# Kernel optimization log

Hardware: AMD Instinct MI355X
Metric: run time of the kernel (lower is better)

The kernel has to match this reference:

```python
import jax, jax.numpy as jnp
import numpy as np

N_NODES = 100000
IN_CH = 256
EMBED = 256
N_EDGES = 300000
EPS = 1e-5


def _glorot(key, shape):
    fan_in, fan_out = shape[0], shape[1]
    lim = (6.0 / (fan_in + fan_out)) ** 0.5
    return jax.random.uniform(key, shape, jnp.float32, -lim, lim)


def setup_inputs() -> dict:
    key = jax.random.key(0)
    ks = jax.random.split(key, 16)
    inp = {}
    inp['node_feat'] = jax.random.normal(ks[0], (N_NODES, IN_CH), jnp.float32)
    inp['src'] = jax.random.randint(ks[1], (N_EDGES,), 0, N_NODES, jnp.int32)
    inp['dst'] = jax.random.randint(ks[2], (N_EDGES,), 0, N_NODES, jnp.int32)
    inp['neg'] = jax.random.randint(ks[3], (N_EDGES,), 0, N_NODES, jnp.int32)
    # GCNConv weights (x @ W + b), 3 layers
    inp['W1'] = _glorot(ks[4], (IN_CH, EMBED)); inp['b1'] = jnp.zeros((EMBED,), jnp.float32)
    inp['W2'] = _glorot(ks[5], (EMBED, EMBED)); inp['b2'] = jnp.zeros((EMBED,), jnp.float32)
    inp['W3'] = _glorot(ks[6], (EMBED, EMBED)); inp['b3'] = jnp.zeros((EMBED,), jnp.float32)
    # BatchNorm affine params (2 BN layers)
    inp['g1'] = jnp.ones((EMBED,), jnp.float32); inp['be1'] = jnp.zeros((EMBED,), jnp.float32)
    inp['g2'] = jnp.ones((EMBED,), jnp.float32); inp['be2'] = jnp.zeros((EMBED,), jnp.float32)
    # LinkPredictor MLP
    inp['fc1_w'] = _glorot(ks[7], (2 * EMBED, EMBED)); inp['fc1_b'] = jnp.zeros((EMBED,), jnp.float32)
    inp['fc2_w'] = _glorot(ks[8], (EMBED, 1)); inp['fc2_b'] = jnp.zeros((1,), jnp.float32)
    return inp


def gcn_conv(x, W, b, src, dst, n):
    # PyG GCNConv: out = D^{-1/2} (A + I) D^{-1/2} (x @ W) + b
    xw = x @ W
    loops = jnp.arange(n, dtype=src.dtype)
    src_l = jnp.concatenate([src, loops])
    dst_l = jnp.concatenate([dst, loops])
    deg = jax.ops.segment_sum(jnp.ones_like(dst_l, jnp.float32), dst_l, num_segments=n)
    dinv = jnp.where(deg > 0, jax.lax.rsqrt(deg), 0.0)
    norm = dinv[src_l] * dinv[dst_l]  # [E+N]
    msg = norm[:, None] * xw[src_l]   # [E+N, d]
    out = jax.ops.segment_sum(msg, dst_l, num_segments=n)
    return out + b


def batch_norm(x, g, b):
    # training-mode BN over node dim, biased variance (torch semantics)
    mu = jnp.mean(x, axis=0)
    var = jnp.mean((x - mu) ** 2, axis=0)
    return (x - mu) * jax.lax.rsqrt(var + EPS) * g + b


def link_pred(z_a, z_b, fc1_w, fc1_b, fc2_w, fc2_b):
    h = jnp.concatenate([z_a, z_b], axis=1) @ fc1_w + fc1_b
    h = jax.nn.relu(h)
    return jax.nn.sigmoid(h @ fc2_w + fc2_b).reshape(-1)


def reference(node_feat, src, dst, neg, W1, b1, W2, b2, W3, b3, g1, be1, g2, be2, fc1_w, fc1_b, fc2_w, fc2_b):
    n = node_feat.shape[0]
    # encoder (dropout p used only in training; inference/deterministic here)
    x = gcn_conv(node_feat, W1, b1, src, dst, n)
    x = jax.nn.relu(batch_norm(x, g1, be1))
    x = gcn_conv(x, W2, b2, src, dst, n)
    x = jax.nn.relu(batch_norm(x, g2, be2))
    z = gcn_conv(x, W3, b3, src, dst, n)
    z_src, z_dst, z_neg = z[src], z[dst], z[neg]
    pos_out = link_pred(z_src, z_dst, fc1_w, fc1_b, fc2_w, fc2_b)
    neg_out = link_pred(z_src, z_neg, fc1_w, fc1_b, fc2_w, fc2_b)
    return (pos_out, neg_out)
```

## Files before the change

kernel.cpp:

```cpp
#include <hip/hip_runtime.h>
#include <hip/hip_bf16.h>

#define N_NODES 100000
#define N_EDGES 300000
#define CH 256
#define EPS 1e-5f
#define AGG_BLOCKS 3125
#define Y_TILES 782
#define Y_TILES_PAD 784

typedef __hip_bfloat16 bf16;
typedef __attribute__((ext_vector_type(8))) short bf16x8_t;
typedef __attribute__((ext_vector_type(4))) float f32x4_t;

__device__ __forceinline__ unsigned short f2bf(float f) {
    bf16 h = __float2bfloat16(f);
    return __builtin_bit_cast(unsigned short, h);
}
__device__ __forceinline__ float bf2f(unsigned short u) {
    unsigned int x = ((unsigned int)u) << 16;
    return __builtin_bit_cast(float, x);
}
__device__ __forceinline__ float bflo(unsigned int w) {
    return __builtin_bit_cast(float, w << 16);
}
__device__ __forceinline__ float bfhi(unsigned int w) {
    return __builtin_bit_cast(float, w & 0xffff0000u);
}
__device__ __forceinline__ unsigned pack2(float a, float b) {
    return (unsigned)f2bf(a) | ((unsigned)f2bf(b) << 16);
}
__device__ __forceinline__ void store_val(bf16* p, float v) { *p = __float2bfloat16(v); }

__device__ __forceinline__ void async_copy16(const void* g, void* l) {
    __builtin_amdgcn_global_load_lds((const __attribute__((address_space(1))) void*)g,
                                     (__attribute__((address_space(3))) void*)l, 16, 0, 0);
}

__global__ void k_zero_int(int* __restrict__ p, int n) {
    int i = blockIdx.x * 256 + threadIdx.x;
    if (i < n) p[i] = 0;
}
__global__ void k_count_deg(const int* __restrict__ dst, int* __restrict__ deg) {
    int e = blockIdx.x * 256 + threadIdx.x;
    if (e < N_EDGES) atomicAdd(&deg[dst[e]], 1);
}
__global__ void k_dinv_from_deg(const int* __restrict__ deg, float* __restrict__ dinv) {
    int i = blockIdx.x * 256 + threadIdx.x;
    if (i < N_NODES) dinv[i] = rsqrtf((float)(deg[i] + 1));
}
__global__ void k_block_sums(const int* __restrict__ deg, int* __restrict__ bsum) {
    __shared__ int s[256];
    int t = threadIdx.x;
    int i = blockIdx.x * 256 + t;
    s[t] = (i < N_NODES) ? deg[i] : 0;
    __syncthreads();
    for (int off = 128; off > 0; off >>= 1) {
        if (t < off) s[t] += s[t + off];
        __syncthreads();
    }
    if (t == 0) bsum[blockIdx.x] = s[0];
}
__global__ void k_scan_bsums(int* __restrict__ bsum, int nb) {
    __shared__ int s[512];
    int t = threadIdx.x;
    int v = (t < nb) ? bsum[t] : 0;
    s[t] = v;
    __syncthreads();
    for (int off = 1; off < 512; off <<= 1) {
        int u = (t >= off) ? s[t - off] : 0;
        __syncthreads();
        s[t] += u;
        __syncthreads();
    }
    if (t < nb) bsum[t] = s[t] - v;
}
__global__ void k_row_ptr(const int* __restrict__ deg, const int* __restrict__ bsum,
                          int* __restrict__ row_ptr) {
    __shared__ int s[256];
    int t = threadIdx.x;
    int i = blockIdx.x * 256 + t;
    int v = (i < N_NODES) ? deg[i] : 0;
    s[t] = v;
    __syncthreads();
    for (int off = 1; off < 256; off <<= 1) {
        int u = (t >= off) ? s[t - off] : 0;
        __syncthreads();
        s[t] += u;
        __syncthreads();
    }
    if (i < N_NODES) row_ptr[i] = bsum[blockIdx.x] + s[t] - v;
    if (blockIdx.x == 0 && t == 0) row_ptr[N_NODES] = N_EDGES;
}
__global__ void k_scatter(const int* __restrict__ src, const int* __restrict__ dst,
                          const int* __restrict__ row_ptr, int* __restrict__ cursor,
                          const float* __restrict__ dinv,
                          int* __restrict__ col, float* __restrict__ wedge,
                          int* __restrict__ eid, int* __restrict__ rowid) {
    int e = blockIdx.x * 256 + threadIdx.x;
    if (e < N_EDGES) {
        int d = dst[e], s = src[e];
        int p = atomicAdd(&cursor[d], 1);
        int idx = row_ptr[d] + p;
        col[idx] = s;
        wedge[idx] = dinv[d] * dinv[s];
        eid[idx] = e;
        rowid[idx] = d;
    }
}

__global__ void k_transpose_all(const float* __restrict__ W1, const float* __restrict__ W2,
                                const float* __restrict__ W3, const float* __restrict__ fc1w,
                                bf16* __restrict__ wt) {
    int which = blockIdx.x >> 8;
    int idx = ((blockIdx.x & 255) << 8) + threadIdx.x;
    int n = idx >> 8, k = idx & 255;
    const float* W; int ro = 0;
    switch (which) {
        case 0: W = W1; break;
        case 1: W = W2; break;
        case 2: W = W3; break;
        case 3: W = fc1w; break;
        default: W = fc1w; ro = 256; break;
    }
    wt[(size_t)which * 65536 + (size_t)n * 256 + k] =
        __float2bfloat16(W[(size_t)(ro + k) * 256 + n]);
}

__global__ void k_cast_bf16_v4(const float* __restrict__ x, unsigned short* __restrict__ y) {
    int i = blockIdx.x * 256 + threadIdx.x;
    float4 v = ((const float4*)x)[i];
    ushort4 o;
    o.x = f2bf(v.x); o.y = f2bf(v.y); o.z = f2bf(v.z); o.w = f2bf(v.w);
    ((ushort4*)y)[i] = o;
}
__global__ void k_bn_relu_bf16(unsigned short* __restrict__ x, const float* __restrict__ scale,
                               const float* __restrict__ shift) {
    int i = blockIdx.x * 256 + threadIdx.x;
    ushort4 m = ((ushort4*)x)[i];
    int c = (i & 63) * 4;
    float4 sc = *(const float4*)(scale + c);
    float4 sh = *(const float4*)(shift + c);
    ushort4 o;
    o.x = f2bf(fmaxf(bf2f(m.x) * sc.x + sh.x, 0.f));
    o.y = f2bf(fmaxf(bf2f(m.y) * sc.y + sh.y, 0.f));
    o.z = f2bf(fmaxf(bf2f(m.z) * sc.z + sh.z, 0.f));
    o.w = f2bf(fmaxf(bf2f(m.w) * sc.w + sh.w, 0.f));
    ((ushort4*)x)[i] = o;
}

template <int NX, bool BIAS>
__global__ __launch_bounds__(256) void k_gemm_mfma(const bf16* __restrict__ A,
                                                   const bf16* __restrict__ Bt,
                                                   bf16* __restrict__ C, int M, int ldc,
                                                   const float* __restrict__ bias256) {
    constexpr int LOG2NX = (NX == 4) ? 2 : 1;
    int id = blockIdx.x;
    int rg = (id & 7) + 8 * (id >> (3 + LOG2NX));
    int ct = (id >> 3) & (NX - 1);
    if (rg >= Y_TILES) return;
    const int row0 = rg * 128;
    const int col0 = ct * 128;

    __shared__ bf16 As[128 * 64];
    __shared__ bf16 Bs[128 * 64];
    const int tid = threadIdx.x;
    const int lane = tid & 63;
    const int w = tid >> 6;
    const int wr = w >> 1, wc = w & 1;
    const int lr = lane & 15, quad = lane >> 4;

    f32x4_t acc[4][4] = {};

    for (int k0 = 0; k0 < 256; k0 += 64) {
#pragma unroll
        for (int i = 0; i < 4; ++i) {
            int j = i * 256 + tid;
            int r = j >> 3, c = j & 7;
            int gk = ((c ^ (r & 7)) << 3);
            int gr = row0 + r; gr = gr < M ? gr : M - 1;
            async_copy16(A + (size_t)gr * 256 + k0 + gk, (void*)(As + j * 8));
            async_copy16(Bt + (size_t)(col0 + r) * 256 + k0 + gk, (void*)(Bs + j * 8));
        }
        __syncthreads();
#pragma unroll
        for (int ks = 0; ks < 2; ++ks) {
            bf16x8_t af[4], bfr[4];
#pragma unroll
            for (int mi = 0; mi < 4; ++mi) {
                int m = wr * 64 + mi * 16 + lr;
                int c = (ks * 4 + quad) ^ (m & 7);
                af[mi] = *(const bf16x8_t*)(As + m * 64 + c * 8);
            }
#pragma unroll
            for (int ni = 0; ni < 4; ++ni) {
                int n = wc * 64 + ni * 16 + lr;
                int c = (ks * 4 + quad) ^ (n & 7);
                bfr[ni] = *(const bf16x8_t*)(Bs + n * 64 + c * 8);
            }
#pragma unroll
            for (int mi = 0; mi < 4; ++mi)
#pragma unroll
                for (int ni = 0; ni < 4; ++ni)
                    acc[mi][ni] = __builtin_amdgcn_mfma_f32_16x16x32_bf16(
                        af[mi], bfr[ni], acc[mi][ni], 0, 0, 0);
        }
        __syncthreads();
    }
    float bv[4];
#pragma unroll
    for (int ni = 0; ni < 4; ++ni) {
        int colg = col0 + wc * 64 + ni * 16 + lr;
        bv[ni] = (BIAS && colg < 256) ? bias256[colg] : 0.f;
    }
#pragma unroll
    for (int mi = 0; mi < 4; ++mi) {
#pragma unroll
        for (int r = 0; r < 4; ++r) {
            int row = row0 + wr * 64 + mi * 16 + quad * 4 + r;
            if (row < M) {
#pragma unroll
                for (int ni = 0; ni < 4; ++ni) {
                    int colg = col0 + wc * 64 + ni * 16 + lr;
                    store_val(C + (size_t)row * ldc + colg, acc[mi][ni][r] + bv[ni]);
                }
            }
        }
    }
}

template <bool STATS>
__global__ __launch_bounds__(256) void k_agg_csr(const unsigned short* __restrict__ xw,
                                                 const int* __restrict__ row_ptr,
                                                 const int* __restrict__ col,
                                                 const float* __restrict__ wedge,
                                                 const float* __restrict__ dinv,
                                                 const float* __restrict__ bias,
                                                 bf16* __restrict__ out,
                                                 float* __restrict__ part) {
    __shared__ float sred[8][256];
    __shared__ float qred[8][256];
    int g = threadIdx.x >> 5, lh = threadIdx.x & 31;
    int base = blockIdx.x * 32 + g * 4;
    const uint4* xwv = (const uint4*)xw;
    float4 b0 = ((const float4*)bias)[lh * 2];
    float4 b1 = ((const float4*)bias)[lh * 2 + 1];
    float s8[8] = {}, q8[8] = {};
#pragma unroll
    for (int n = 0; n < 4; ++n) {
        int node = base + n;
        int beg = row_ptr[node], end = row_ptr[node + 1];
        float dv = dinv[node];
        uint4 xr = xwv[(size_t)node * 32 + lh];
        float s2 = dv * dv;
        float a0 = s2 * bflo(xr.x), a1 = s2 * bfhi(xr.x);
        float a2 = s2 * bflo(xr.y), a3 = s2 * bfhi(xr.y);
        float a4 = s2 * bflo(xr.z), a5 = s2 * bfhi(xr.z);
        float a6 = s2 * bflo(xr.w), a7 = s2 * bfhi(xr.w);
        int i = beg;
        for (; i + 2 <= end; i += 2) {
            int sa = col[i], sb = col[i + 1];
            float wa = wedge[i], wb = wedge[i + 1];
            uint4 ma = xwv[(size_t)sa * 32 + lh];
            uint4 mb = xwv[(size_t)sb * 32 + lh];
            a0 += wa * bflo(ma.x) + wb * bflo(mb.x);
            a1 += wa * bfhi(ma.x) + wb * bfhi(mb.x);
            a2 += wa * bflo(ma.y) + wb * bflo(mb.y);
            a3 += wa * bfhi(ma.y) + wb * bfhi(mb.y);
            a4 += wa * bflo(ma.z) + wb * bflo(mb.z);
            a5 += wa * bfhi(ma.z) + wb * bfhi(mb.z);
            a6 += wa * bflo(ma.w) + wb * bflo(mb.w);
            a7 += wa * bfhi(ma.w) + wb * bfhi(mb.w);
        }
        if (i < end) {
            int sa = col[i];
            float wa = wedge[i];
            uint4 ma = xwv[(size_t)sa * 32 + lh];
            a0 += wa * bflo(ma.x); a1 += wa * bfhi(ma.x);
            a2 += wa * bflo(ma.y); a3 += wa * bfhi(ma.y);
            a4 += wa * bflo(ma.z); a5 += wa * bfhi(ma.z);
            a6 += wa * bflo(ma.w); a7 += wa * bfhi(ma.w);
        }
        a0 += b0.x; a1 += b0.y; a2 += b0.z; a3 += b0.w;
        a4 += b1.x; a5 += b1.y; a6 += b1.z; a7 += b1.w;
        uint4 o;
        o.x = pack2(a0, a1); o.y = pack2(a2, a3);
        o.z = pack2(a4, a5); o.w = pack2(a6, a7);
        ((uint4*)(out + (size_t)node * CH))[lh] = o;
        if (STATS) {
            s8[0] += a0; s8[1] += a1; s8[2] += a2; s8[3] += a3;
            s8[4] += a4; s8[5] += a5; s8[6] += a6; s8[7] += a7;
            q8[0] += a0 * a0; q8[1] += a1 * a1; q8[2] += a2 * a2; q8[3] += a3 * a3;
            q8[4] += a4 * a4; q8[5] += a5 * a5; q8[6] += a6 * a6; q8[7] += a7 * a7;
        }
    }
    if (STATS) {
#pragma unroll
        for (int j = 0; j < 8; ++j) {
            sred[g][lh * 8 + j] = s8[j];
            qred[g][lh * 8 + j] = q8[j];
        }
        __syncthreads();
        int t = threadIdx.x;
        float ss = 0.f, qq = 0.f;
#pragma unroll
        for (int gg = 0; gg < 8; ++gg) {
            ss += sred[gg][t];
            qq += qred[gg][t];
        }
        part[(size_t)blockIdx.x * 512 + t] = ss;
        part[(size_t)blockIdx.x * 512 + 256 + t] = qq;
    }
}

__global__ __launch_bounds__(256) void k_bn_finalize(const float* __restrict__ part,
                                                     const float* __restrict__ g,
                                                     const float* __restrict__ be,
                                                     float* __restrict__ scale,
                                                     float* __restrict__ shift) {
    int wave = threadIdx.x >> 6, lane = threadIdx.x & 63;
    int c = blockIdx.x * 4 + wave;
    float s = 0.f, q = 0.f;
    for (int j = lane; j < AGG_BLOCKS; j += 64) {
        s += part[(size_t)j * 512 + c];
        q += part[(size_t)j * 512 + 256 + c];
    }
#pragma unroll
    for (int off = 32; off > 0; off >>= 1) {
        s += __shfl_down(s, off, 64);
        q += __shfl_down(q, off, 64);
    }
    if (lane == 0) {
        float mu = s * (1.0f / N_NODES);
        float var = q * (1.0f / N_NODES) - mu * mu;
        float sc = g[c] * rsqrtf(var + EPS);
        scale[c] = sc;
        shift[c] = be[c] - mu * sc;
    }
}

__global__ __launch_bounds__(256) void k_edge_score(
        const unsigned short* __restrict__ uv,
        const int* __restrict__ col, const int* __restrict__ eid,
        const int* __restrict__ rowid, const int* __restrict__ neg,
        const float* __restrict__ fc2_w, const float* __restrict__ fc2_b,
        float* __restrict__ out) {
    constexpr int NWG = 18750;
    constexpr int Q = NWG / 8, R = NWG % 8;
    int bid = blockIdx.x;
    int xcd = bid & 7, ord = bid >> 3;
    int swz = ((xcd < R) ? xcd * (Q + 1) : R * (Q + 1) + (xcd - R) * Q) + ord;
    int wave = threadIdx.x >> 6, lane = threadIdx.x & 63;
    int qtr = lane >> 4, l = lane & 15;
    int i = swz * 16 + wave * 4 + qtr;
    int s = col[i], d = rowid[i], e = eid[i];
    int g = neg[e];
    const uint4* uvv = (const uint4*)uv;
    uint4 u0 = uvv[(size_t)s * 64 + l * 2];
    uint4 u1 = uvv[(size_t)s * 64 + l * 2 + 1];
    uint4 p0 = uvv[(size_t)d * 64 + 32 + l * 2];
    uint4 p1 = uvv[(size_t)d * 64 + 33 + l * 2];
    uint4 n0 = uvv[(size_t)g * 64 + 32 + l * 2];
    uint4 n1 = uvv[(size_t)g * 64 + 33 + l * 2];
    float4 w0 = ((const float4*)fc2_w)[l * 4];
    float4 w1 = ((const float4*)fc2_w)[l * 4 + 1];
    float4 w2 = ((const float4*)fc2_w)[l * 4 + 2];
    float4 w3 = ((const float4*)fc2_w)[l * 4 + 3];

    float t0 = bflo(u0.x), t1 = bfhi(u0.x), t2 = bflo(u0.y), t3 = bfhi(u0.y);
    float t4 = bflo(u0.z), t5 = bfhi(u0.z), t6 = bflo(u0.w), t7 = bfhi(u0.w);
    float t8 = bflo(u1.x), t9 = bfhi(u1.x), ta = bflo(u1.y), tb = bfhi(u1.y);
    float tc = bflo(u1.z), td = bfhi(u1.z), te = bflo(u1.w), tf = bfhi(u1.w);

    float accp =
        fmaxf(t0 + bflo(p0.x), 0.f) * w0.x + fmaxf(t1 + bfhi(p0.x), 0.f) * w0.y +
        fmaxf(t2 + bflo(p0.y), 0.f) * w0.z + fmaxf(t3 + bfhi(p0.y), 0.f) * w0.w +
        fmaxf(t4 + bflo(p0.z), 0.f) * w1.x + fmaxf(t5 + bfhi(p0.z), 0.f) * w1.y +
        fmaxf(t6 + bflo(p0.w), 0.f) * w1.z + fmaxf(t7 + bfhi(p0.w), 0.f) * w1.w +
        fmaxf(t8 + bflo(p1.x), 0.f) * w2.x + fmaxf(t9 + bfhi(p1.x), 0.f) * w2.y +
        fmaxf(ta + bflo(p1.y), 0.f) * w2.z + fmaxf(tb + bfhi(p1.y), 0.f) * w2.w +
        fmaxf(tc + bflo(p1.z), 0.f) * w3.x + fmaxf(td + bfhi(p1.z), 0.f) * w3.y +
        fmaxf(te + bflo(p1.w), 0.f) * w3.z + fmaxf(tf + bfhi(p1.w), 0.f) * w3.w;
    float accn =
        fmaxf(t0 + bflo(n0.x), 0.f) * w0.x + fmaxf(t1 + bfhi(n0.x), 0.f) * w0.y +
        fmaxf(t2 + bflo(n0.y), 0.f) * w0.z + fmaxf(t3 + bfhi(n0.y), 0.f) * w0.w +
        fmaxf(t4 + bflo(n0.z), 0.f) * w1.x + fmaxf(t5 + bfhi(n0.z), 0.f) * w1.y +
        fmaxf(t6 + bflo(n0.w), 0.f) * w1.z + fmaxf(t7 + bfhi(n0.w), 0.f) * w1.w +
        fmaxf(t8 + bflo(n1.x), 0.f) * w2.x + fmaxf(t9 + bfhi(n1.x), 0.f) * w2.y +
        fmaxf(ta + bflo(n1.y), 0.f) * w2.z + fmaxf(tb + bfhi(n1.y), 0.f) * w2.w +
        fmaxf(tc + bflo(n1.z), 0.f) * w3.x + fmaxf(td + bfhi(n1.z), 0.f) * w3.y +
        fmaxf(te + bflo(n1.w), 0.f) * w3.z + fmaxf(tf + bfhi(n1.w), 0.f) * w3.w;
#pragma unroll
    for (int off = 8; off > 0; off >>= 1) {
        accp += __shfl_down(accp, off, 64);
        accn += __shfl_down(accn, off, 64);
    }
    if (l == 0) {
        float bb = fc2_b[0];
        out[e] = 1.0f / (1.0f + expf(-(accp + bb)));
        out[N_EDGES + e] = 1.0f / (1.0f + expf(-(accn + bb)));
    }
}

extern "C" void kernel_launch(void* const* d_in, const int* in_sizes, int n_in,
                              void* d_out, int out_size, void* d_ws, size_t ws_size,
                              hipStream_t stream) {
    const float* node_feat = (const float*)d_in[0];
    const int* src = (const int*)d_in[1];
    const int* dst = (const int*)d_in[2];
    const int* neg = (const int*)d_in[3];
    const float* W1 = (const float*)d_in[4];  const float* b1 = (const float*)d_in[5];
    const float* W2 = (const float*)d_in[6];  const float* b2 = (const float*)d_in[7];
    const float* W3 = (const float*)d_in[8];  const float* b3 = (const float*)d_in[9];
    const float* g1 = (const float*)d_in[10]; const float* be1 = (const float*)d_in[11];
    const float* g2 = (const float*)d_in[12]; const float* be2 = (const float*)d_in[13];
    const float* fc1_w = (const float*)d_in[14]; const float* fc1_b = (const float*)d_in[15];
    const float* fc2_w = (const float*)d_in[16]; const float* fc2_b = (const float*)d_in[17];
    float* out = (float*)d_out;

    const size_t NF = (size_t)N_NODES * CH;
    bf16* UV = (bf16*)d_ws;
    bf16* Xbf = UV + 2 * NF;
    bf16* XwBf = Xbf + NF;
    bf16* wt = XwBf + NF;
    float* dinv = (float*)(wt + 5 * 65536);
    float* bnpart = dinv + N_NODES;
    float* scale = bnpart + (size_t)AGG_BLOCKS * 512;
    float* shift = scale + CH;
    float* wedge = shift + CH;
    int* ideg = (int*)(wedge + N_EDGES);
    int* cursor = ideg + N_NODES;
    int* row_ptr = cursor + N_NODES;
    int* col = row_ptr + N_NODES + 1;
    int* eid = col + N_EDGES;
    int* rowid = eid + N_EDGES;
    int* bsum = rowid + N_EDGES;
    (void)ws_size;

    int gemmBlocks = 2 * Y_TILES_PAD;
    int uvBlocks = 4 * Y_TILES_PAD;
    int nodeBlocks = (N_NODES + 255) / 256;
    int edgeBlocks = (N_EDGES + 255) / 256;
    int v4Blocks = (int)(NF / 4 / 256);
    int scoreBlocks = N_EDGES / 16;

    k_zero_int<<<(2 * N_NODES + 255) / 256, 256, 0, stream>>>(ideg, 2 * N_NODES);
    k_count_deg<<<edgeBlocks, 256, 0, stream>>>(dst, ideg);
    k_dinv_from_deg<<<nodeBlocks, 256, 0, stream>>>(ideg, dinv);
    k_block_sums<<<nodeBlocks, 256, 0, stream>>>(ideg, bsum);
    k_scan_bsums<<<1, 512, 0, stream>>>(bsum, nodeBlocks);
    k_row_ptr<<<nodeBlocks, 256, 0, stream>>>(ideg, bsum, row_ptr);
    k_scatter<<<edgeBlocks, 256, 0, stream>>>(src, dst, row_ptr, cursor, dinv, col, wedge,
                                              eid, rowid);

    k_transpose_all<<<1280, 256, 0, stream>>>(W1, W2, W3, fc1_w, wt);

    k_cast_bf16_v4<<<v4Blocks, 256, 0, stream>>>(node_feat, (unsigned short*)Xbf);
    k_gemm_mfma<2, false><<<gemmBlocks, 256, 0, stream>>>(Xbf, wt, XwBf, N_NODES, 256, nullptr);
    k_agg_csr<true><<<AGG_BLOCKS, 256, 0, stream>>>((unsigned short*)XwBf, row_ptr, col,
                                                    wedge, dinv, b1, Xbf, bnpart);
    k_bn_finalize<<<64, 256, 0, stream>>>(bnpart, g1, be1, scale, shift);
    k_bn_relu_bf16<<<v4Blocks, 256, 0, stream>>>((unsigned short*)Xbf, scale, shift);

    k_gemm_mfma<2, false><<<gemmBlocks, 256, 0, stream>>>(Xbf, wt + 65536, XwBf, N_NODES, 256, nullptr);
    k_agg_csr<true><<<AGG_BLOCKS, 256, 0, stream>>>((unsigned short*)XwBf, row_ptr, col,
                                                    wedge, dinv, b2, Xbf, bnpart);
    k_bn_finalize<<<64, 256, 0, stream>>>(bnpart, g2, be2, scale, shift);
    k_bn_relu_bf16<<<v4Blocks, 256, 0, stream>>>((unsigned short*)Xbf, scale, shift);

    k_gemm_mfma<2, false><<<gemmBlocks, 256, 0, stream>>>(Xbf, wt + 2 * 65536, XwBf, N_NODES, 256, nullptr);
    k_agg_csr<false><<<AGG_BLOCKS, 256, 0, stream>>>((unsigned short*)XwBf, row_ptr, col,
                                                     wedge, dinv, b3, Xbf, nullptr);

    k_gemm_mfma<4, true><<<uvBlocks, 256, 0, stream>>>(Xbf, wt + 3 * 65536, UV, N_NODES, 512, fc1_b);
    k_edge_score<<<scoreBlocks, 256, 0, stream>>>((unsigned short*)UV, col, eid, rowid, neg,
                                                  fc2_w, fc2_b, out);
}
```

Baseline: 632.5 us.

## Aggregate before GEMM, fuse BN stats into GEMM, fold W3 into fc1

Reorders each GCN layer to aggregate raw features first and then multiply by W, using linearity of the normalized adjacency. BatchNorm statistics are now computed in the GEMM epilogue, and the BN+ReLU is applied on the fly while gathering in the next aggregation, which removes the separate bn_relu pass. W3 is pre-multiplied into fc1 (and b3 folded into the bias), so the third GEMM and the UV GEMM become a single GEMM. The goal is fewer full passes over the 100k x 256 activations. In exchange, BN+ReLU is recomputed for every gathered neighbor and the different bf16 rounding order may shift numerics slightly.

```diff
diff --git a/kernel.cpp b/kernel.cpp
--- a/kernel.cpp
+++ b/kernel.cpp
@@ -110,21 +110,40 @@
 }
 
 __global__ void k_transpose_all(const float* __restrict__ W1, const float* __restrict__ W2,
-                                const float* __restrict__ W3, const float* __restrict__ fc1w,
                                 bf16* __restrict__ wt) {
     int which = blockIdx.x >> 8;
     int idx = ((blockIdx.x & 255) << 8) + threadIdx.x;
     int n = idx >> 8, k = idx & 255;
-    const float* W; int ro = 0;
-    switch (which) {
-        case 0: W = W1; break;
-        case 1: W = W2; break;
-        case 2: W = W3; break;
-        case 3: W = fc1w; break;
-        default: W = fc1w; ro = 256; break;
-    }
+    const float* W = which ? W2 : W1;
     wt[(size_t)which * 65536 + (size_t)n * 256 + k] =
-        __float2bfloat16(W[(size_t)(ro + k) * 256 + n]);
+        __float2bfloat16(W[(size_t)k * 256 + n]);
+}
+
+__global__ void k_fuse_w(const float* __restrict__ W3, const float* __restrict__ fc1w,
+                         bf16* __restrict__ wtf) {
+    __shared__ float w3row[256];
+    int k = blockIdx.x;
+    int n = threadIdx.x;
+    if (n < 256) w3row[n] = W3[(size_t)k * 256 + n];
+    __syncthreads();
+    int nc = n & 255;
+    size_t ro = (n < 256) ? 0 : 256;
+    float acc = 0.f;
+#pragma unroll 4
+    for (int j = 0; j < 256; ++j)
+        acc += w3row[j] * fc1w[(ro + j) * 256 + nc];
+    wtf[(size_t)n * 256 + k] = __float2bfloat16(acc);
+}
+__global__ void k_fuse_bias(const float* __restrict__ b3, const float* __restrict__ fc1w,
+                            const float* __restrict__ fc1b, float* __restrict__ bout) {
+    int n = threadIdx.x;
+    int nc = n & 255;
+    size_t ro = (n < 256) ? 0 : 256;
+    float acc = (n < 256) ? fc1b[n] : 0.f;
+#pragma unroll 4
+    for (int j = 0; j < 256; ++j)
+        acc += b3[j] * fc1w[(ro + j) * 256 + nc];
+    bout[n] = acc;
 }
 
 __global__ void k_cast_bf16_v4(const float* __restrict__ x, unsigned short* __restrict__ y) {
@@ -134,26 +153,13 @@
     o.x = f2bf(v.x); o.y = f2bf(v.y); o.z = f2bf(v.z); o.w = f2bf(v.w);
     ((ushort4*)y)[i] = o;
 }
-__global__ void k_bn_relu_bf16(unsigned short* __restrict__ x, const float* __restrict__ scale,
-                               const float* __restrict__ shift) {
-    int i = blockIdx.x * 256 + threadIdx.x;
-    ushort4 m = ((ushort4*)x)[i];
-    int c = (i & 63) * 4;
-    float4 sc = *(const float4*)(scale + c);
-    float4 sh = *(const float4*)(shift + c);
-    ushort4 o;
-    o.x = f2bf(fmaxf(bf2f(m.x) * sc.x + sh.x, 0.f));
-    o.y = f2bf(fmaxf(bf2f(m.y) * sc.y + sh.y, 0.f));
-    o.z = f2bf(fmaxf(bf2f(m.z) * sc.z + sh.z, 0.f));
-    o.w = f2bf(fmaxf(bf2f(m.w) * sc.w + sh.w, 0.f));
-    ((ushort4*)x)[i] = o;
-}
-
-template <int NX, bool BIAS>
+
+template <int NX, bool BIAS, bool STATS>
 __global__ __launch_bounds__(256) void k_gemm_mfma(const bf16* __restrict__ A,
                                                    const bf16* __restrict__ Bt,
                                                    bf16* __restrict__ C, int M, int ldc,
-                                                   const float* __restrict__ bias256) {
+                                                   const float* __restrict__ bias,
+                                                   float* __restrict__ part) {
     constexpr int LOG2NX = (NX == 4) ? 2 : 1;
     int id = blockIdx.x;
     int rg = (id & 7) + 8 * (id >> (3 + LOG2NX));
@@ -164,6 +170,8 @@
 
     __shared__ bf16 As[128 * 64];
     __shared__ bf16 Bs[128 * 64];
+    __shared__ float sS[2][128];
+    __shared__ float sQ[2][128];
     const int tid = threadIdx.x;
     const int lane = tid & 63;
     const int w = tid >> 6;
@@ -207,11 +215,54 @@
         }
         __syncthreads();
     }
-    float bv[4];
 #pragma unroll
     for (int ni = 0; ni < 4; ++ni) {
         int colg = col0 + wc * 64 + ni * 16 + lr;
-        bv[ni] = (BIAS && colg < 256) ? bias256[colg] : 0.f;
+        float bv = BIAS ? bias[colg] : 0.f;
+#pragma unroll
+        for (int mi = 0; mi < 4; ++mi)
+#pragma unroll
+            for (int r = 0; r < 4; ++r) acc[mi][ni][r] += bv;
+    }
+    if (STATS) {
+        float cs[4] = {}, cq[4] = {};
+#pragma unroll
+        for (int mi = 0; mi < 4; ++mi)
+#pragma unroll
+            for (int r = 0; r < 4; ++r) {
+                int row = row0 + wr * 64 + mi * 16 + quad * 4 + r;
+                if (row < M) {
+#pragma unroll
+                    for (int ni = 0; ni < 4; ++ni) {
+                        float v = acc[mi][ni][r];
+                        cs[ni] += v;
+                        cq[ni] += v * v;
+                    }
+                }
+            }
+#pragma unroll
+        for (int ni = 0; ni < 4; ++ni) {
+            cs[ni] += __shfl_xor(cs[ni], 16, 64);
+            cs[ni] += __shfl_xor(cs[ni], 32, 64);
+            cq[ni] += __shfl_xor(cq[ni], 16, 64);
+            cq[ni] += __shfl_xor(cq[ni], 32, 64);
+        }
+        if (quad == 0) {
+#pragma unroll
+            for (int ni = 0; ni < 4; ++ni) {
+                int cc = wc * 64 + ni * 16 + lr;
+                sS[wr][cc] = cs[ni];
+                sQ[wr][cc] = cq[ni];
+            }
+        }
+        __syncthreads();
+        if (tid < 128) {
+            float ss = sS[0][tid] + sS[1][tid];
+            float qq = sQ[0][tid] + sQ[1][tid];
+            int cg = col0 + tid;
+            part[(size_t)rg * 512 + cg] = ss;
+            part[(size_t)rg * 512 + 256 + cg] = qq;
+        }
     }
 #pragma unroll
     for (int mi = 0; mi < 4; ++mi) {
@@ -222,94 +273,83 @@
 #pragma unroll
                 for (int ni = 0; ni < 4; ++ni) {
                     int colg = col0 + wc * 64 + ni * 16 + lr;
-                    store_val(C + (size_t)row * ldc + colg, acc[mi][ni][r] + bv[ni]);
+                    store_val(C + (size_t)row * ldc + colg, acc[mi][ni][r]);
                 }
             }
         }
     }
 }
 
-template <bool STATS>
-__global__ __launch_bounds__(256) void k_agg_csr(const unsigned short* __restrict__ xw,
+template <bool BN>
+__device__ __forceinline__ void expand8(uint4 m, const float* sc, const float* sh, float* r) {
+    r[0] = bflo(m.x); r[1] = bfhi(m.x); r[2] = bflo(m.y); r[3] = bfhi(m.y);
+    r[4] = bflo(m.z); r[5] = bfhi(m.z); r[6] = bflo(m.w); r[7] = bfhi(m.w);
+    if (BN) {
+#pragma unroll
+        for (int i = 0; i < 8; ++i) r[i] = fmaxf(r[i] * sc[i] + sh[i], 0.f);
+    }
+}
+
+template <bool BN>
+__global__ __launch_bounds__(256) void k_agg_csr(const unsigned short* __restrict__ x,
                                                  const int* __restrict__ row_ptr,
                                                  const int* __restrict__ col,
                                                  const float* __restrict__ wedge,
                                                  const float* __restrict__ dinv,
-                                                 const float* __restrict__ bias,
-                                                 bf16* __restrict__ out,
-                                                 float* __restrict__ part) {
-    __shared__ float sred[8][256];
-    __shared__ float qred[8][256];
+                                                 const float* __restrict__ scale,
+                                                 const float* __restrict__ shift,
+                                                 bf16* __restrict__ out) {
     int g = threadIdx.x >> 5, lh = threadIdx.x & 31;
     int base = blockIdx.x * 32 + g * 4;
-    const uint4* xwv = (const uint4*)xw;
-    float4 b0 = ((const float4*)bias)[lh * 2];
-    float4 b1 = ((const float4*)bias)[lh * 2 + 1];
-    float s8[8] = {}, q8[8] = {};
+    const uint4* xv = (const uint4*)x;
+    float sc[8], sh[8];
+    if (BN) {
+        float4 a = ((const float4*)scale)[lh * 2];
+        float4 b = ((const float4*)scale)[lh * 2 + 1];
+        float4 c = ((const float4*)shift)[lh * 2];
+        float4 d = ((const float4*)shift)[lh * 2 + 1];
+        sc[0] = a.x; sc[1] = a.y; sc[2] = a.z; sc[3] = a.w;
+        sc[4] = b.x; sc[5] = b.y; sc[6] = b.z; sc[7] = b.w;
+        sh[0] = c.x; sh[1] = c.y; sh[2] = c.z; sh[3] = c.w;
+        sh[4] = d.x; sh[5] = d.y; sh[6] = d.z; sh[7] = d.w;
+    }
 #pragma unroll
     for (int n = 0; n < 4; ++n) {
         int node = base + n;
         int beg = row_ptr[node], end = row_ptr[node + 1];
         float dv = dinv[node];
-        uint4 xr = xwv[(size_t)node * 32 + lh];
         float s2 = dv * dv;
-        float a0 = s2 * bflo(xr.x), a1 = s2 * bfhi(xr.x);
-        float a2 = s2 * bflo(xr.y), a3 = s2 * bfhi(xr.y);
-        float a4 = s2 * bflo(xr.z), a5 = s2 * bfhi(xr.z);
-        float a6 = s2 * bflo(xr.w), a7 = s2 * bfhi(xr.w);
+        uint4 xr = xv[(size_t)node * 32 + lh];
+        float rs[8];
+        expand8<BN>(xr, sc, sh, rs);
+        float a[8];
+#pragma unroll
+        for (int t = 0; t < 8; ++t) a[t] = s2 * rs[t];
         int i = beg;
         for (; i + 2 <= end; i += 2) {
             int sa = col[i], sb = col[i + 1];
             float wa = wedge[i], wb = wedge[i + 1];
-            uint4 ma = xwv[(size_t)sa * 32 + lh];
-            uint4 mb = xwv[(size_t)sb * 32 + lh];
-            a0 += wa * bflo(ma.x) + wb * bflo(mb.x);
-            a1 += wa * bfhi(ma.x) + wb * bfhi(mb.x);
-            a2 += wa * bflo(ma.y) + wb * bflo(mb.y);
-            a3 += wa * bfhi(ma.y) + wb * bfhi(mb.y);
-            a4 += wa * bflo(ma.z) + wb * bflo(mb.z);
-            a5 += wa * bfhi(ma.z) + wb * bfhi(mb.z);
-            a6 += wa * bflo(ma.w) + wb * bflo(mb.w);
-            a7 += wa * bfhi(ma.w) + wb * bfhi(mb.w);
+            uint4 ma = xv[(size_t)sa * 32 + lh];
+            uint4 mb = xv[(size_t)sb * 32 + lh];
+            float ra[8], rb[8];
+            expand8<BN>(ma, sc, sh, ra);
+            expand8<BN>(mb, sc, sh, rb);
+#pragma unroll
+            for (int t = 0; t < 8; ++t) a[t] += wa * ra[t] + wb * rb[t];
         }
         if (i < end) {
             int sa = col[i];
             float wa = wedge[i];
-            uint4 ma = xwv[(size_t)sa * 32 + lh];
-            a0 += wa * bflo(ma.x); a1 += wa * bfhi(ma.x);
-            a2 += wa * bflo(ma.y); a3 += wa * bfhi(ma.y);
-            a4 += wa * bflo(ma.z); a5 += wa * bfhi(ma.z);
-            a6 += wa * bflo(ma.w); a7 += wa * bfhi(ma.w);
-        }
-        a0 += b0.x; a1 += b0.y; a2 += b0.z; a3 += b0.w;
-        a4 += b1.x; a5 += b1.y; a6 += b1.z; a7 += b1.w;
+            uint4 ma = xv[(size_t)sa * 32 + lh];
+            float ra[8];
+            expand8<BN>(ma, sc, sh, ra);
+#pragma unroll
+            for (int t = 0; t < 8; ++t) a[t] += wa * ra[t];
+        }
         uint4 o;
-        o.x = pack2(a0, a1); o.y = pack2(a2, a3);
-        o.z = pack2(a4, a5); o.w = pack2(a6, a7);
+        o.x = pack2(a[0], a[1]); o.y = pack2(a[2], a[3]);
+        o.z = pack2(a[4], a[5]); o.w = pack2(a[6], a[7]);
         ((uint4*)(out + (size_t)node * CH))[lh] = o;
-        if (STATS) {
-            s8[0] += a0; s8[1] += a1; s8[2] += a2; s8[3] += a3;
-            s8[4] += a4; s8[5] += a5; s8[6] += a6; s8[7] += a7;
-            q8[0] += a0 * a0; q8[1] += a1 * a1; q8[2] += a2 * a2; q8[3] += a3 * a3;
-            q8[4] += a4 * a4; q8[5] += a5 * a5; q8[6] += a6 * a6; q8[7] += a7 * a7;
-        }
-    }
-    if (STATS) {
-#pragma unroll
-        for (int j = 0; j < 8; ++j) {
-            sred[g][lh * 8 + j] = s8[j];
-            qred[g][lh * 8 + j] = q8[j];
-        }
-        __syncthreads();
-        int t = threadIdx.x;
-        float ss = 0.f, qq = 0.f;
-#pragma unroll
-        for (int gg = 0; gg < 8; ++gg) {
-            ss += sred[gg][t];
-            qq += qred[gg][t];
-        }
-        part[(size_t)blockIdx.x * 512 + t] = ss;
-        part[(size_t)blockIdx.x * 512 + 256 + t] = qq;
     }
 }
 
@@ -321,7 +361,7 @@
     int wave = threadIdx.x >> 6, lane = threadIdx.x & 63;
     int c = blockIdx.x * 4 + wave;
     float s = 0.f, q = 0.f;
-    for (int j = lane; j < AGG_BLOCKS; j += 64) {
+    for (int j = lane; j < Y_TILES; j += 64) {
         s += part[(size_t)j * 512 + c];
         q += part[(size_t)j * 512 + 256 + c];
     }
@@ -423,11 +463,12 @@
     bf16* Xbf = UV + 2 * NF;
     bf16* XwBf = Xbf + NF;
     bf16* wt = XwBf + NF;
-    float* dinv = (float*)(wt + 5 * 65536);
+    float* dinv = (float*)(wt + 4 * 65536);
     float* bnpart = dinv + N_NODES;
-    float* scale = bnpart + (size_t)AGG_BLOCKS * 512;
+    float* scale = bnpart + (size_t)Y_TILES * 512;
     float* shift = scale + CH;
-    float* wedge = shift + CH;
+    float* b3fc = shift + CH;
+    float* wedge = b3fc + 512;
     int* ideg = (int*)(wedge + N_EDGES);
     int* cursor = ideg + N_NODES;
     int* row_ptr = cursor + N_NODES;
@@ -453,26 +494,29 @@
     k_scatter<<<edgeBlocks, 256, 0, stream>>>(src, dst, row_ptr, cursor, dinv, col, wedge,
                                               eid, rowid);
 
-    k_transpose_all<<<1280, 256, 0, stream>>>(W1, W2, W3, fc1_w, wt);
+    k_transpose_all<<<512, 256, 0, stream>>>(W1, W2, wt);
+    k_fuse_w<<<256, 512, 0, stream>>>(W3, fc1_w, wt + 2 * 65536);
+    k_fuse_bias<<<1, 512, 0, stream>>>(b3, fc1_w, fc1_b, b3fc);
 
     k_cast_bf16_v4<<<v4Blocks, 256, 0, stream>>>(node_feat, (unsigned short*)Xbf);
-    k_gemm_mfma<2, false><<<gemmBlocks, 256, 0, stream>>>(Xbf, wt, XwBf, N_NODES, 256, nullptr);
-    k_agg_csr<true><<<AGG_BLOCKS, 256, 0, stream>>>((unsigned short*)XwBf, row_ptr, col,
-                                                    wedge, dinv, b1, Xbf, bnpart);
+
+    k_agg_csr<false><<<AGG_BLOCKS, 256, 0, stream>>>((unsigned short*)Xbf, row_ptr, col,
+                                                     wedge, dinv, nullptr, nullptr, XwBf);
+    k_gemm_mfma<2, true, true><<<gemmBlocks, 256, 0, stream>>>(XwBf, wt, Xbf, N_NODES, 256,
+                                                               b1, bnpart);
     k_bn_finalize<<<64, 256, 0, stream>>>(bnpart, g1, be1, scale, shift);
-    k_bn_relu_bf16<<<v4Blocks, 256, 0, stream>>>((unsigned short*)Xbf, scale, shift);
-
-    k_gemm_mfma<2, false><<<gemmBlocks, 256, 0, stream>>>(Xbf, wt + 65536, XwBf, N_NODES, 256, nullptr);
-    k_agg_csr<true><<<AGG_BLOCKS, 256, 0, stream>>>((unsigned short*)XwBf, row_ptr, col,
-                                                    wedge, dinv, b2, Xbf, bnpart);
+
+    k_agg_csr<true><<<AGG_BLOCKS, 256, 0, stream>>>((unsigned short*)Xbf, row_ptr, col,
+                                                    wedge, dinv, scale, shift, XwBf);
+    k_gemm_mfma<2, true, true><<<gemmBlocks, 256, 0, stream>>>(XwBf, wt + 65536, Xbf,
+                                                               N_NODES, 256, b2, bnpart);
     k_bn_finalize<<<64, 256, 0, stream>>>(bnpart, g2, be2, scale, shift);
-    k_bn_relu_bf16<<<v4Blocks, 256, 0, stream>>>((unsigned short*)Xbf, scale, shift);
-
-    k_gemm_mfma<2, false><<<gemmBlocks, 256, 0, stream>>>(Xbf, wt + 2 * 65536, XwBf, N_NODES, 256, nullptr);
-    k_agg_csr<false><<<AGG_BLOCKS, 256, 0, stream>>>((unsigned short*)XwBf, row_ptr, col,
-                                                     wedge, dinv, b3, Xbf, nullptr);
-
-    k_gemm_mfma<4, true><<<uvBlocks, 256, 0, stream>>>(Xbf, wt + 3 * 65536, UV, N_NODES, 512, fc1_b);
+
+    k_agg_csr<true><<<AGG_BLOCKS, 256, 0, stream>>>((unsigned short*)Xbf, row_ptr, col,
+                                                    wedge, dinv, scale, shift, XwBf);
+    k_gemm_mfma<4, true, false><<<uvBlocks, 256, 0, stream>>>(XwBf, wt + 2 * 65536, UV,
+                                                              N_NODES, 512, b3fc, nullptr);
+
     k_edge_score<<<scoreBlocks, 256, 0, stream>>>((unsigned short*)UV, col, eid, rowid, neg,
                                                   fc2_w, fc2_b, out);
 }
```

Measured after the change: 566.0 us. 10.5% less time.
